# Kernel optimization log

Hardware: AMD Instinct MI355X
Metric: run time of the kernel (lower is better)

The kernel has to match this reference:

```python
import jax, jax.numpy as jnp
from jax import lax
import numpy as np

B, S, H = 4, 4096, 1024
NH, HD, L = 8, 128, 64
EPS = 1e-8


def setup_inputs() -> dict:
    key = jax.random.key(0)
    ks = jax.random.split(key, 11)
    std = 0.02
    d = NH * HD
    return {
        "f_in": jax.random.normal(ks[0], (B, S, H), jnp.float32),
        "i_in": jax.random.normal(ks[1], (B, S, H), jnp.float32),
        "z_in": jax.random.normal(ks[2], (B, S, H), jnp.float32),
        "o_in": jax.random.normal(ks[3], (B, S, H), jnp.float32),
        "c0": jax.random.normal(ks[4], (B, NH, HD), jnp.float32),
        "h0": jax.random.normal(ks[5], (B, NH, HD), jnp.float32),
        "Wf": jax.random.normal(ks[6], (d, H), jnp.float32) * std,
        "bf": jnp.zeros((d,), jnp.float32),
        "Wi": jax.random.normal(ks[7], (d, H), jnp.float32) * std,
        "bi": jnp.zeros((d,), jnp.float32),
        "Wz": jax.random.normal(ks[8], (d, H), jnp.float32) * std,
        "bz": jnp.zeros((d,), jnp.float32),
        "Wo": jax.random.normal(ks[9], (d, H), jnp.float32) * std,
        "bo": jnp.zeros((d,), jnp.float32),
        "Wp": jax.random.normal(ks[10], (H, d), jnp.float32) * std,
        "bp": jnp.zeros((H,), jnp.float32),
    }


def _to_blocks(x):
    # (B,S,NH*HD) -> (n_blocks, B, NH, HD, L)
    nb = S // L
    return x.reshape(B, nb, L, NH, HD).transpose(1, 0, 3, 4, 2)


def reference(f_in, i_in, z_in, o_in, c0, h0, Wf, bf, Wi, bi, Wz, bz, Wo, bo, Wp, bp):
    fx = _to_blocks(f_in @ Wf.T + bf)
    ix = _to_blocks(i_in @ Wi.T + bi)
    zx = _to_blocks(z_in @ Wz.T + bz)
    ox = _to_blocks(o_in @ Wo.T + bo)

    f = jax.nn.sigmoid(fx + 1.0)            # (nb,B,NH,HD,L)
    o = jax.nn.sigmoid(ox)
    upd = jax.nn.sigmoid(ix) * jnp.tanh(zx)

    k = jnp.arange(L)[:, None]
    l = jnp.arange(L + 1)[None, :]
    ones_mask = l >= k + 1                   # set to 1 before cumulative log-prod
    zeros_mask = l >= k + 2                  # strictly-future entries zeroed

    def block_step(c, blk):
        fb, ub, ob = blk                     # each (B,NH,HD,L)
        cf = jnp.concatenate(
            [fb, jnp.ones(fb.shape[:3] + (1,), fb.dtype)], axis=3)  # (B,NH,HD,L+1)
        Fm = jnp.broadcast_to(cf[:, :, :, None, :], fb.shape[:3] + (L, L + 1))
        Fm = jnp.where(ones_mask, 1.0, Fm)
        # reverse cumulative product in log space (matches torch eps trick)
        Fm = jnp.exp(jnp.flip(jnp.cumsum(jnp.flip(jnp.log(Fm + EPS), -1), -1), -1)) - EPS
        Fm = jnp.where(zeros_mask, 0.0, Fm)  # (B,NH,HD,L,L+1)
        u = jnp.concatenate([c[..., None], ub], axis=3)  # (B,NH,HD,L+1)
        cs = jnp.einsum('bhdkl,bhdl->bhdk', Fm, u)       # (B,NH,HD,L)
        hs = ob * jnp.tanh(cs)
        return cs[..., -1], hs

    last_c, hs = lax.scan(block_step, c0, (f, upd, o))   # hs: (nb,B,NH,HD,L)
    last_h = hs[-1][..., -1]
    y = hs.transpose(1, 0, 4, 2, 3).reshape(B, S, NH * HD)
    y = y @ Wp.T + bp                                    # (B,S,H)
    return y, last_c, last_h
```

## Files before the change

### kernel.cpp

```cpp
#include <hip/hip_runtime.h>
#include <hip/hip_bf16.h>
#include <type_traits>

#define GATE_ELEMS 16777216ull
#define W_ELEMS    1048576ull

typedef float f32x4 __attribute__((ext_vector_type(4)));
typedef short s16x8 __attribute__((ext_vector_type(8)));
typedef unsigned short u16;

__device__ __forceinline__ u16 f2bf(float f) {
  union { float f; unsigned u; } v; v.f = f;
  unsigned r = v.u + 0x7fffu + ((v.u >> 16) & 1u);
  return (u16)(r >> 16);
}
__device__ __forceinline__ float bf2f(u16 u) {
  union { unsigned u; float f; } v; v.u = ((unsigned)u) << 16;
  return v.f;
}
__device__ __forceinline__ float sigmoidf_(float x) {
  return 1.0f / (1.0f + __expf(-x));
}
__device__ __forceinline__ float tanhf_(float x) {
  x = fminf(fmaxf(x, -15.f), 15.f);
  const float e = __expf(2.f * x);
  return (e - 1.f) / (e + 1.f);
}

__device__ __forceinline__ void load_lds16(const u16* g, u16* l) {
  __builtin_amdgcn_global_load_lds(
      (const __attribute__((address_space(1))) unsigned int*)g,
      (__attribute__((address_space(3))) unsigned int*)l, 16, 0, 0);
}

#define XCHUNKS 8388608u
#define WCHUNKS 655360u
__global__ void cvt_all(const float* __restrict__ x0, const float* __restrict__ x1,
                        const float* __restrict__ x2, const float* __restrict__ x3,
                        const float* __restrict__ w0, const float* __restrict__ w1,
                        const float* __restrict__ w2, const float* __restrict__ w3,
                        const float* __restrict__ w4,
                        u16* __restrict__ xdst, u16* __restrict__ wdst) {
  const unsigned total = XCHUNKS + WCHUNKS;
  for (unsigned i = blockIdx.x * 256 + threadIdx.x; i < total; i += 2048 * 256) {
    const float* s; u16* d; size_t loc;
    if (i < XCHUNKS) {
      const int w = i >> 21;
      loc = (size_t)(i & 2097151u) * 8;
      s = (w == 0) ? x0 : (w == 1) ? x1 : (w == 2) ? x2 : x3;
      d = xdst + (size_t)w * GATE_ELEMS;
    } else {
      const unsigned j = i - XCHUNKS;
      const int w = j >> 17;
      loc = (size_t)(j & 131071u) * 8;
      s = (w == 0) ? w0 : (w == 1) ? w1 : (w == 2) ? w2 : (w == 3) ? w3 : w4;
      d = wdst + (size_t)w * W_ELEMS;
    }
    const float4 a = *reinterpret_cast<const float4*>(s + loc);
    const float4 b = *reinterpret_cast<const float4*>(s + loc + 4);
    s16x8 wv;
    wv[0] = (short)f2bf(a.x); wv[1] = (short)f2bf(a.y);
    wv[2] = (short)f2bf(a.z); wv[3] = (short)f2bf(a.w);
    wv[4] = (short)f2bf(b.x); wv[5] = (short)f2bf(b.y);
    wv[6] = (short)f2bf(b.z); wv[7] = (short)f2bf(b.w);
    *reinterpret_cast<s16x8*>(d + loc) = wv;
  }
}

__device__ __forceinline__ void stage_mat(const u16* __restrict__ M, int R0, int kt,
                                          u16* ldsbase, int tid) {
#pragma unroll
  for (int l = 0; l < 4; ++l) {
    const int T  = l * 256 + tid;
    const int r  = T >> 3;
    const int sl = (T & 7) ^ (r & 7);
    load_lds16(M + (size_t)(R0 + r) * 1024 + kt + sl * 8,
               ldsbase + (T & ~63) * 8);
  }
}

template <typename OT>
__global__ __launch_bounds__(256, 2)
void gemm_bt128(const u16* __restrict__ A, const u16* __restrict__ Bm,
                const float* __restrict__ bias, OT* __restrict__ C) {
  extern __shared__ u16 lds[];
  const int tid  = threadIdx.x;
  const int lane = tid & 63;
  const int wave = tid >> 6;
  const int wr = wave >> 1;
  const int wc = wave & 1;
  const int frow = lane & 15;
  const int kq   = lane >> 4;

  int bid = blockIdx.x;
  bid = (bid & 7) * 128 + (bid >> 3);
  const int m0 = (bid >> 3) * 128;
  const int n0 = (bid & 7) * 128;

  f32x4 acc[4][4];
#pragma unroll
  for (int i = 0; i < 4; ++i)
#pragma unroll
    for (int j = 0; j < 4; ++j)
      acc[i][j] = (f32x4){0.f, 0.f, 0.f, 0.f};

  stage_mat(A,  m0, 0, lds,        tid);
  stage_mat(Bm, n0, 0, lds + 8192, tid);
  __syncthreads();

  int cur = 0;
#pragma unroll 2
  for (int t = 0; t < 16; ++t) {
    if (t < 15) {
      u16* nb = lds + (cur ^ 1) * 16384;
      stage_mat(A,  m0, (t + 1) * 64, nb,        tid);
      stage_mat(Bm, n0, (t + 1) * 64, nb + 8192, tid);
    }
    const u16* Ab = lds + cur * 16384;
    const u16* Bb = Ab + 8192;
#pragma unroll
    for (int kk = 0; kk < 2; ++kk) {
      s16x8 a[4], b[4];
#pragma unroll
      for (int mf = 0; mf < 4; ++mf) {
        const int r  = wr * 64 + mf * 16 + frow;
        const int ps = (kk * 4 + kq) ^ (r & 7);
        a[mf] = *reinterpret_cast<const s16x8*>(&Ab[r * 64 + ps * 8]);
      }
#pragma unroll
      for (int nf = 0; nf < 4; ++nf) {
        const int r  = wc * 64 + nf * 16 + frow;
        const int ps = (kk * 4 + kq) ^ (r & 7);
        b[nf] = *reinterpret_cast<const s16x8*>(&Bb[r * 64 + ps * 8]);
      }
#pragma unroll
      for (int mf = 0; mf < 4; ++mf)
#pragma unroll
        for (int nf = 0; nf < 4; ++nf)
          acc[mf][nf] = __builtin_amdgcn_mfma_f32_16x16x32_bf16(a[mf], b[nf], acc[mf][nf], 0, 0, 0);
    }
    __syncthreads();
    cur ^= 1;
  }

#pragma unroll
  for (int nf = 0; nf < 4; ++nf) {
    const int col = n0 + wc * 64 + nf * 16 + frow;
    const float bv = bias[col];
#pragma unroll
    for (int mf = 0; mf < 4; ++mf) {
      const int rbase = m0 + wr * 64 + mf * 16 + kq * 4;
#pragma unroll
      for (int r = 0; r < 4; ++r) {
        const float v = acc[mf][nf][r] + bv;
        if constexpr (std::is_same<OT, float>::value)
          C[(size_t)(rbase + r) * 1024 + col] = v;
        else
          C[(size_t)(rbase + r) * 1024 + col] = f2bf(v);
      }
    }
  }
}

__global__ void scan_pass1(const u16* __restrict__ fx, const u16* __restrict__ ix,
                           const u16* __restrict__ zx,
                           float* __restrict__ P, float* __restrict__ cl) {
  const int t  = blockIdx.x * 256 + threadIdx.x;
  const int jg = (t & 255) * 4;
  const int q  = (t >> 8) & 63;
  const int b  = t >> 14;
  const size_t base = ((size_t)(b * 4096 + q * 64)) * 1024 + jg;
  float Pp[4] = {1.f, 1.f, 1.f, 1.f};
  float c[4]  = {0.f, 0.f, 0.f, 0.f};
  for (int s = 0; s < 64; ++s) {
    const size_t o = base + (size_t)s * 1024;
    const ushort4 fv = *reinterpret_cast<const ushort4*>(fx + o);
    const ushort4 iv = *reinterpret_cast<const ushort4*>(ix + o);
    const ushort4 zv = *reinterpret_cast<const ushort4*>(zx + o);
    const u16* fp = (const u16*)&fv;
    const u16* ip = (const u16*)&iv;
    const u16* zp = (const u16*)&zv;
#pragma unroll
    for (int k = 0; k < 4; ++k) {
      const float f = sigmoidf_(bf2f(fp[k]) + 1.f);
      const float u = sigmoidf_(bf2f(ip[k])) * tanhf_(bf2f(zp[k]));
      Pp[k] *= f;
      c[k] = f * c[k] + u;
    }
  }
  const int sidx = q * 4096 + b * 1024 + jg;
  *reinterpret_cast<float4*>(P + sidx)  = make_float4(Pp[0], Pp[1], Pp[2], Pp[3]);
  *reinterpret_cast<float4*>(cl + sidx) = make_float4(c[0], c[1], c[2], c[3]);
}

__global__ void scan_pass2(const float* __restrict__ P, const float* __restrict__ cl,
                           const float* __restrict__ c0, float* __restrict__ cin,
                           float* __restrict__ lastc) {
  const int idx = blockIdx.x * 256 + threadIdx.x;
  float carry = c0[idx];
#pragma unroll
  for (int q = 0; q < 64; ++q) {
    const int s = q * 4096 + idx;
    cin[s] = carry;
    carry = fmaf(P[s], carry, cl[s]);
  }
  lastc[idx] = carry;
}

__global__ void scan_pass3(const u16* __restrict__ fx, const u16* __restrict__ ix,
                           const u16* __restrict__ zx, const u16* __restrict__ ox,
                           const float* __restrict__ cin,
                           u16* __restrict__ h, float* __restrict__ lasth) {
  const int t  = blockIdx.x * 256 + threadIdx.x;
  const int jg = (t & 255) * 4;
  const int q  = (t >> 8) & 63;
  const int b  = t >> 14;
  const size_t base = ((size_t)(b * 4096 + q * 64)) * 1024 + jg;
  const float4 ci = *reinterpret_cast<const float4*>(cin + q * 4096 + b * 1024 + jg);
  float c[4]  = {ci.x, ci.y, ci.z, ci.w};
  float hv[4] = {0.f, 0.f, 0.f, 0.f};
  for (int s = 0; s < 64; ++s) {
    const size_t o = base + (size_t)s * 1024;
    const ushort4 fv = *reinterpret_cast<const ushort4*>(fx + o);
    const ushort4 iv = *reinterpret_cast<const ushort4*>(ix + o);
    const ushort4 zv = *reinterpret_cast<const ushort4*>(zx + o);
    const ushort4 ov = *reinterpret_cast<const ushort4*>(ox + o);
    const u16* fp = (const u16*)&fv;
    const u16* ip = (const u16*)&iv;
    const u16* zp = (const u16*)&zv;
    const u16* op = (const u16*)&ov;
    ushort4 hw;
    u16* hp = (u16*)&hw;
#pragma unroll
    for (int k = 0; k < 4; ++k) {
      const float f = sigmoidf_(bf2f(fp[k]) + 1.f);
      const float u = sigmoidf_(bf2f(ip[k])) * tanhf_(bf2f(zp[k]));
      c[k] = f * c[k] + u;
      hv[k] = sigmoidf_(bf2f(op[k])) * tanhf_(c[k]);
      hp[k] = f2bf(hv[k]);
    }
    *reinterpret_cast<ushort4*>(h + o) = hw;
  }
  if (q == 63)
    *reinterpret_cast<float4*>(lasth + b * 1024 + jg) =
        make_float4(hv[0], hv[1], hv[2], hv[3]);
}

extern "C" void kernel_launch(void* const* d_in, const int* in_sizes, int n_in,
                              void* d_out, int out_size, void* d_ws, size_t ws_size,
                              hipStream_t stream) {
  const float* xin[4]  = {(const float*)d_in[0], (const float*)d_in[1],
                          (const float*)d_in[2], (const float*)d_in[3]};
  const float* c0      = (const float*)d_in[4];
  const float* W[5]    = {(const float*)d_in[6], (const float*)d_in[8],
                          (const float*)d_in[10], (const float*)d_in[12],
                          (const float*)d_in[14]};
  const float* bias[5] = {(const float*)d_in[7], (const float*)d_in[9],
                          (const float*)d_in[11], (const float*)d_in[13],
                          (const float*)d_in[15]};
  float* out = (float*)d_out;

  (void)hipFuncSetAttribute((const void*)gemm_bt128<u16>,
                            hipFuncAttributeMaxDynamicSharedMemorySize, 65536);
  (void)hipFuncSetAttribute((const void*)gemm_bt128<float>,
                            hipFuncAttributeMaxDynamicSharedMemorySize, 65536);

  u16* xbf = (u16*)d_ws;
  u16* wbf = xbf + 4 * GATE_ELEMS;
  float* Pbuf   = (float*)(wbf + 5 * W_ELEMS);
  float* clbuf  = Pbuf + 262144;
  float* cinbuf = clbuf + 262144;

  u16* gp[4];
  gp[0] = (u16*)d_out;
  gp[1] = xbf;
  gp[2] = xbf + GATE_ELEMS;
  gp[3] = xbf + 2 * GATE_ELEMS;
  u16* h = xbf + 3 * GATE_ELEMS;

  cvt_all<<<2048, 256, 0, stream>>>(xin[0], xin[1], xin[2], xin[3],
                                    W[0], W[1], W[2], W[3], W[4], xbf, wbf);

  for (int g = 0; g < 4; ++g)
    gemm_bt128<u16><<<1024, 256, 65536, stream>>>(
        xbf + (size_t)g * GATE_ELEMS, wbf + (size_t)g * W_ELEMS, bias[g], gp[g]);

  scan_pass1<<<256, 256, 0, stream>>>(gp[0], gp[1], gp[2], Pbuf, clbuf);
  scan_pass2<<<16, 256, 0, stream>>>(Pbuf, clbuf, c0, cinbuf, out + GATE_ELEMS);
  scan_pass3<<<256, 256, 0, stream>>>(gp[0], gp[1], gp[2], gp[3], cinbuf, h,
                                      out + GATE_ELEMS + 4096);

  gemm_bt128<float><<<1024, 256, 65536, stream>>>(h, wbf + 4 * W_ELEMS, bias[4], out);
}
```

Baseline: 677.6 us.

## Fuse fp32-to-bf16 activation conversion into gate GEMM and deepen scan parallelism

The separate conversion pass over the four fp32 activation tensors is removed. The gate GEMM now loads fp32 A tiles into registers, converts them with a packed bf16 instruction, and writes them to LDS, overlapping this with the MFMA work on the current tile. This avoids writing and re-reading a 128MB bf16 copy. The scan passes split the sequence into 128 chunks instead of 64 and keep an 8-deep register prefetch ring, giving more parallelism and latency hiding; the cost is more register pressure in the GEMM and a longer serial pass2.

```diff
diff --git a/kernel.cpp b/kernel.cpp
--- a/kernel.cpp
+++ b/kernel.cpp
@@ -4,6 +4,7 @@
 
 #define GATE_ELEMS 16777216ull
 #define W_ELEMS    1048576ull
+#define NQ 128
 
 typedef float f32x4 __attribute__((ext_vector_type(4)));
 typedef short s16x8 __attribute__((ext_vector_type(8)));
@@ -26,49 +27,34 @@
   const float e = __expf(2.f * x);
   return (e - 1.f) / (e + 1.f);
 }
-
+__device__ __forceinline__ unsigned cvtpk(float lo, float hi) {
+  unsigned r;
+  asm("v_cvt_pk_bf16_f32 %0, %1, %2" : "=v"(r) : "v"(lo), "v"(hi));
+  return r;
+}
 __device__ __forceinline__ void load_lds16(const u16* g, u16* l) {
   __builtin_amdgcn_global_load_lds(
       (const __attribute__((address_space(1))) unsigned int*)g,
       (__attribute__((address_space(3))) unsigned int*)l, 16, 0, 0);
 }
 
-#define XCHUNKS 8388608u
-#define WCHUNKS 655360u
-__global__ void cvt_all(const float* __restrict__ x0, const float* __restrict__ x1,
-                        const float* __restrict__ x2, const float* __restrict__ x3,
-                        const float* __restrict__ w0, const float* __restrict__ w1,
-                        const float* __restrict__ w2, const float* __restrict__ w3,
-                        const float* __restrict__ w4,
-                        u16* __restrict__ xdst, u16* __restrict__ wdst) {
-  const unsigned total = XCHUNKS + WCHUNKS;
-  for (unsigned i = blockIdx.x * 256 + threadIdx.x; i < total; i += 2048 * 256) {
-    const float* s; u16* d; size_t loc;
-    if (i < XCHUNKS) {
-      const int w = i >> 21;
-      loc = (size_t)(i & 2097151u) * 8;
-      s = (w == 0) ? x0 : (w == 1) ? x1 : (w == 2) ? x2 : x3;
-      d = xdst + (size_t)w * GATE_ELEMS;
-    } else {
-      const unsigned j = i - XCHUNKS;
-      const int w = j >> 17;
-      loc = (size_t)(j & 131071u) * 8;
-      s = (w == 0) ? w0 : (w == 1) ? w1 : (w == 2) ? w2 : (w == 3) ? w3 : w4;
-      d = wdst + (size_t)w * W_ELEMS;
-    }
-    const float4 a = *reinterpret_cast<const float4*>(s + loc);
-    const float4 b = *reinterpret_cast<const float4*>(s + loc + 4);
-    s16x8 wv;
-    wv[0] = (short)f2bf(a.x); wv[1] = (short)f2bf(a.y);
-    wv[2] = (short)f2bf(a.z); wv[3] = (short)f2bf(a.w);
-    wv[4] = (short)f2bf(b.x); wv[5] = (short)f2bf(b.y);
-    wv[6] = (short)f2bf(b.z); wv[7] = (short)f2bf(b.w);
-    *reinterpret_cast<s16x8*>(d + loc) = wv;
-  }
-}
-
-__device__ __forceinline__ void stage_mat(const u16* __restrict__ M, int R0, int kt,
-                                          u16* ldsbase, int tid) {
+__global__ void cvt_w_kernel(const float* __restrict__ w0, const float* __restrict__ w1,
+                             const float* __restrict__ w2, const float* __restrict__ w3,
+                             const float* __restrict__ w4, u16* __restrict__ dst) {
+  const float* src = (blockIdx.y == 0) ? w0 : (blockIdx.y == 1) ? w1
+                   : (blockIdx.y == 2) ? w2 : (blockIdx.y == 3) ? w3 : w4;
+  u16* d = dst + (size_t)blockIdx.y * W_ELEMS;
+  const size_t i = ((size_t)blockIdx.x * 256 + threadIdx.x) * 8;
+  const float4 a = *reinterpret_cast<const float4*>(src + i);
+  const float4 b = *reinterpret_cast<const float4*>(src + i + 4);
+  uint4 q;
+  q.x = cvtpk(a.x, a.y); q.y = cvtpk(a.z, a.w);
+  q.z = cvtpk(b.x, b.y); q.w = cvtpk(b.z, b.w);
+  *reinterpret_cast<uint4*>(d + i) = q;
+}
+
+__device__ __forceinline__ void stage_bf16(const u16* __restrict__ M, int R0, int kt,
+                                           u16* ldsbase, int tid) {
 #pragma unroll
   for (int l = 0; l < 4; ++l) {
     const int T  = l * 256 + tid;
@@ -78,34 +64,128 @@
                ldsbase + (T & ~63) * 8);
   }
 }
-
-template <typename OT>
+__device__ __forceinline__ void a_issue(const float* __restrict__ A, int m0, int kt,
+                                        int tid, float4 (&av)[8]) {
+  const float* p = A + (size_t)(m0 + (tid >> 3)) * 1024 + kt + (tid & 7) * 8;
+#pragma unroll
+  for (int l = 0; l < 4; ++l) {
+    av[2 * l]     = *reinterpret_cast<const float4*>(p + (size_t)l * 32 * 1024);
+    av[2 * l + 1] = *reinterpret_cast<const float4*>(p + (size_t)l * 32 * 1024 + 4);
+  }
+}
+__device__ __forceinline__ void a_write(u16* Abuf, int tid, const float4 (&av)[8]) {
+  const int rb = tid >> 3, s = tid & 7;
+#pragma unroll
+  for (int l = 0; l < 4; ++l) {
+    const int r  = rb + l * 32;
+    const int ps = s ^ (r & 7);
+    uint4 q;
+    q.x = cvtpk(av[2 * l].x,     av[2 * l].y);
+    q.y = cvtpk(av[2 * l].z,     av[2 * l].w);
+    q.z = cvtpk(av[2 * l + 1].x, av[2 * l + 1].y);
+    q.w = cvtpk(av[2 * l + 1].z, av[2 * l + 1].w);
+    *reinterpret_cast<uint4*>(&Abuf[r * 64 + ps * 8]) = q;
+  }
+}
+
+#define MFMA_BLOCK(Ab, Bb)                                                        \
+  _Pragma("unroll")                                                               \
+  for (int kk = 0; kk < 2; ++kk) {                                                \
+    s16x8 a[4], b[4];                                                             \
+    _Pragma("unroll")                                                             \
+    for (int mf = 0; mf < 4; ++mf) {                                              \
+      const int r  = wr * 64 + mf * 16 + frow;                                    \
+      const int ps = (kk * 4 + kq) ^ (r & 7);                                     \
+      a[mf] = *reinterpret_cast<const s16x8*>(&(Ab)[r * 64 + ps * 8]);            \
+    }                                                                             \
+    _Pragma("unroll")                                                             \
+    for (int nf = 0; nf < 4; ++nf) {                                              \
+      const int r  = wc * 64 + nf * 16 + frow;                                    \
+      const int ps = (kk * 4 + kq) ^ (r & 7);                                     \
+      b[nf] = *reinterpret_cast<const s16x8*>(&(Bb)[r * 64 + ps * 8]);            \
+    }                                                                             \
+    _Pragma("unroll")                                                             \
+    for (int mf = 0; mf < 4; ++mf)                                                \
+      _Pragma("unroll")                                                           \
+      for (int nf = 0; nf < 4; ++nf)                                              \
+        acc[mf][nf] = __builtin_amdgcn_mfma_f32_16x16x32_bf16(a[mf], b[nf],       \
+                                                              acc[mf][nf], 0, 0, 0); \
+  }
+
+#define GEMM_PRE()                                                                \
+  const int tid  = threadIdx.x;                                                   \
+  const int lane = tid & 63;                                                      \
+  const int wave = tid >> 6;                                                      \
+  const int wr = wave >> 1, wc = wave & 1;                                        \
+  const int frow = lane & 15, kq = lane >> 4;                                     \
+  int bid = blockIdx.x;                                                           \
+  bid = (bid & 7) * 128 + (bid >> 3);                                             \
+  const int m0 = (bid >> 3) * 128;                                                \
+  const int n0 = (bid & 7) * 128;                                                 \
+  f32x4 acc[4][4];                                                                \
+  _Pragma("unroll")                                                               \
+  for (int i = 0; i < 4; ++i)                                                     \
+    _Pragma("unroll")                                                             \
+    for (int j = 0; j < 4; ++j)                                                   \
+      acc[i][j] = (f32x4){0.f, 0.f, 0.f, 0.f};
+
+#define GEMM_EPI(C, OT)                                                           \
+  _Pragma("unroll")                                                               \
+  for (int nf = 0; nf < 4; ++nf) {                                                \
+    const int col = n0 + wc * 64 + nf * 16 + frow;                                \
+    const float bv = bias[col];                                                   \
+    _Pragma("unroll")                                                             \
+    for (int mf = 0; mf < 4; ++mf) {                                              \
+      const int rbase = m0 + wr * 64 + mf * 16 + kq * 4;                          \
+      _Pragma("unroll")                                                           \
+      for (int r = 0; r < 4; ++r) {                                               \
+        const float v = acc[mf][nf][r] + bv;                                      \
+        if constexpr (std::is_same<OT, float>::value)                             \
+          (C)[(size_t)(rbase + r) * 1024 + col] = v;                              \
+        else                                                                      \
+          (C)[(size_t)(rbase + r) * 1024 + col] = f2bf(v);                        \
+      }                                                                           \
+    }                                                                             \
+  }
+
 __global__ __launch_bounds__(256, 2)
-void gemm_bt128(const u16* __restrict__ A, const u16* __restrict__ Bm,
-                const float* __restrict__ bias, OT* __restrict__ C) {
+void gemm_gate(const float* __restrict__ A, const u16* __restrict__ Bm,
+               const float* __restrict__ bias, u16* __restrict__ C) {
   extern __shared__ u16 lds[];
-  const int tid  = threadIdx.x;
-  const int lane = tid & 63;
-  const int wave = tid >> 6;
-  const int wr = wave >> 1;
-  const int wc = wave & 1;
-  const int frow = lane & 15;
-  const int kq   = lane >> 4;
-
-  int bid = blockIdx.x;
-  bid = (bid & 7) * 128 + (bid >> 3);
-  const int m0 = (bid >> 3) * 128;
-  const int n0 = (bid & 7) * 128;
-
-  f32x4 acc[4][4];
-#pragma unroll
-  for (int i = 0; i < 4; ++i)
-#pragma unroll
-    for (int j = 0; j < 4; ++j)
-      acc[i][j] = (f32x4){0.f, 0.f, 0.f, 0.f};
-
-  stage_mat(A,  m0, 0, lds,        tid);
-  stage_mat(Bm, n0, 0, lds + 8192, tid);
+  GEMM_PRE();
+
+  float4 av[8];
+  a_issue(A, m0, 0, tid, av);
+  stage_bf16(Bm, n0, 0, lds + 8192, tid);
+  a_write(lds, tid, av);
+  __syncthreads();
+
+  int cur = 0;
+#pragma unroll 2
+  for (int t = 0; t < 16; ++t) {
+    u16* nb = lds + (cur ^ 1) * 16384;
+    if (t < 15) {
+      a_issue(A, m0, (t + 1) * 64, tid, av);
+      stage_bf16(Bm, n0, (t + 1) * 64, nb + 8192, tid);
+    }
+    const u16* Ab = lds + cur * 16384;
+    const u16* Bb = Ab + 8192;
+    MFMA_BLOCK(Ab, Bb);
+    if (t < 15) a_write(nb, tid, av);
+    __syncthreads();
+    cur ^= 1;
+  }
+  GEMM_EPI(C, u16);
+}
+
+__global__ __launch_bounds__(256, 2)
+void gemm_out(const u16* __restrict__ A, const u16* __restrict__ Bm,
+              const float* __restrict__ bias, float* __restrict__ C) {
+  extern __shared__ u16 lds[];
+  GEMM_PRE();
+
+  stage_bf16(A,  m0, 0, lds,        tid);
+  stage_bf16(Bm, n0, 0, lds + 8192, tid);
   __syncthreads();
 
   int cur = 0;
@@ -113,53 +193,16 @@
   for (int t = 0; t < 16; ++t) {
     if (t < 15) {
       u16* nb = lds + (cur ^ 1) * 16384;
-      stage_mat(A,  m0, (t + 1) * 64, nb,        tid);
-      stage_mat(Bm, n0, (t + 1) * 64, nb + 8192, tid);
+      stage_bf16(A,  m0, (t + 1) * 64, nb,        tid);
+      stage_bf16(Bm, n0, (t + 1) * 64, nb + 8192, tid);
     }
     const u16* Ab = lds + cur * 16384;
     const u16* Bb = Ab + 8192;
-#pragma unroll
-    for (int kk = 0; kk < 2; ++kk) {
-      s16x8 a[4], b[4];
-#pragma unroll
-      for (int mf = 0; mf < 4; ++mf) {
-        const int r  = wr * 64 + mf * 16 + frow;
-        const int ps = (kk * 4 + kq) ^ (r & 7);
-        a[mf] = *reinterpret_cast<const s16x8*>(&Ab[r * 64 + ps * 8]);
-      }
-#pragma unroll
-      for (int nf = 0; nf < 4; ++nf) {
-        const int r  = wc * 64 + nf * 16 + frow;
-        const int ps = (kk * 4 + kq) ^ (r & 7);
-        b[nf] = *reinterpret_cast<const s16x8*>(&Bb[r * 64 + ps * 8]);
-      }
-#pragma unroll
-      for (int mf = 0; mf < 4; ++mf)
-#pragma unroll
-        for (int nf = 0; nf < 4; ++nf)
-          acc[mf][nf] = __builtin_amdgcn_mfma_f32_16x16x32_bf16(a[mf], b[nf], acc[mf][nf], 0, 0, 0);
-    }
+    MFMA_BLOCK(Ab, Bb);
     __syncthreads();
     cur ^= 1;
   }
-
-#pragma unroll
-  for (int nf = 0; nf < 4; ++nf) {
-    const int col = n0 + wc * 64 + nf * 16 + frow;
-    const float bv = bias[col];
-#pragma unroll
-    for (int mf = 0; mf < 4; ++mf) {
-      const int rbase = m0 + wr * 64 + mf * 16 + kq * 4;
-#pragma unroll
-      for (int r = 0; r < 4; ++r) {
-        const float v = acc[mf][nf][r] + bv;
-        if constexpr (std::is_same<OT, float>::value)
-          C[(size_t)(rbase + r) * 1024 + col] = v;
-        else
-          C[(size_t)(rbase + r) * 1024 + col] = f2bf(v);
-      }
-    }
-  }
+  GEMM_EPI(C, float);
 }
 
 __global__ void scan_pass1(const u16* __restrict__ fx, const u16* __restrict__ ix,
@@ -167,16 +210,29 @@
                            float* __restrict__ P, float* __restrict__ cl) {
   const int t  = blockIdx.x * 256 + threadIdx.x;
   const int jg = (t & 255) * 4;
-  const int q  = (t >> 8) & 63;
-  const int b  = t >> 14;
-  const size_t base = ((size_t)(b * 4096 + q * 64)) * 1024 + jg;
+  const int q  = (t >> 8) & 127;
+  const int b  = t >> 15;
+  const size_t base = ((size_t)(b * 4096 + q * 32)) * 1024 + jg;
+
+  ushort4 pf[8], pi[8], pz[8];
+#pragma unroll
+  for (int d = 0; d < 8; ++d) {
+    const size_t o = base + (size_t)d * 1024;
+    pf[d] = *reinterpret_cast<const ushort4*>(fx + o);
+    pi[d] = *reinterpret_cast<const ushort4*>(ix + o);
+    pz[d] = *reinterpret_cast<const ushort4*>(zx + o);
+  }
   float Pp[4] = {1.f, 1.f, 1.f, 1.f};
   float c[4]  = {0.f, 0.f, 0.f, 0.f};
-  for (int s = 0; s < 64; ++s) {
-    const size_t o = base + (size_t)s * 1024;
-    const ushort4 fv = *reinterpret_cast<const ushort4*>(fx + o);
-    const ushort4 iv = *reinterpret_cast<const ushort4*>(ix + o);
-    const ushort4 zv = *reinterpret_cast<const ushort4*>(zx + o);
+#pragma unroll
+  for (int s = 0; s < 32; ++s) {
+    const ushort4 fv = pf[s & 7], iv = pi[s & 7], zv = pz[s & 7];
+    if (s + 8 < 32) {
+      const size_t o = base + (size_t)(s + 8) * 1024;
+      pf[s & 7] = *reinterpret_cast<const ushort4*>(fx + o);
+      pi[s & 7] = *reinterpret_cast<const ushort4*>(ix + o);
+      pz[s & 7] = *reinterpret_cast<const ushort4*>(zx + o);
+    }
     const u16* fp = (const u16*)&fv;
     const u16* ip = (const u16*)&iv;
     const u16* zp = (const u16*)&zv;
@@ -198,8 +254,8 @@
                            float* __restrict__ lastc) {
   const int idx = blockIdx.x * 256 + threadIdx.x;
   float carry = c0[idx];
-#pragma unroll
-  for (int q = 0; q < 64; ++q) {
+#pragma unroll 8
+  for (int q = 0; q < NQ; ++q) {
     const int s = q * 4096 + idx;
     cin[s] = carry;
     carry = fmaf(P[s], carry, cl[s]);
@@ -213,18 +269,32 @@
                            u16* __restrict__ h, float* __restrict__ lasth) {
   const int t  = blockIdx.x * 256 + threadIdx.x;
   const int jg = (t & 255) * 4;
-  const int q  = (t >> 8) & 63;
-  const int b  = t >> 14;
-  const size_t base = ((size_t)(b * 4096 + q * 64)) * 1024 + jg;
+  const int q  = (t >> 8) & 127;
+  const int b  = t >> 15;
+  const size_t base = ((size_t)(b * 4096 + q * 32)) * 1024 + jg;
+
+  ushort4 pf[8], pi[8], pz[8], po[8];
+#pragma unroll
+  for (int d = 0; d < 8; ++d) {
+    const size_t o = base + (size_t)d * 1024;
+    pf[d] = *reinterpret_cast<const ushort4*>(fx + o);
+    pi[d] = *reinterpret_cast<const ushort4*>(ix + o);
+    pz[d] = *reinterpret_cast<const ushort4*>(zx + o);
+    po[d] = *reinterpret_cast<const ushort4*>(ox + o);
+  }
   const float4 ci = *reinterpret_cast<const float4*>(cin + q * 4096 + b * 1024 + jg);
   float c[4]  = {ci.x, ci.y, ci.z, ci.w};
   float hv[4] = {0.f, 0.f, 0.f, 0.f};
-  for (int s = 0; s < 64; ++s) {
-    const size_t o = base + (size_t)s * 1024;
-    const ushort4 fv = *reinterpret_cast<const ushort4*>(fx + o);
-    const ushort4 iv = *reinterpret_cast<const ushort4*>(ix + o);
-    const ushort4 zv = *reinterpret_cast<const ushort4*>(zx + o);
-    const ushort4 ov = *reinterpret_cast<const ushort4*>(ox + o);
+#pragma unroll
+  for (int s = 0; s < 32; ++s) {
+    const ushort4 fv = pf[s & 7], iv = pi[s & 7], zv = pz[s & 7], ov = po[s & 7];
+    if (s + 8 < 32) {
+      const size_t o = base + (size_t)(s + 8) * 1024;
+      pf[s & 7] = *reinterpret_cast<const ushort4*>(fx + o);
+      pi[s & 7] = *reinterpret_cast<const ushort4*>(ix + o);
+      pz[s & 7] = *reinterpret_cast<const ushort4*>(zx + o);
+      po[s & 7] = *reinterpret_cast<const ushort4*>(ox + o);
+    }
     const u16* fp = (const u16*)&fv;
     const u16* ip = (const u16*)&iv;
     const u16* zp = (const u16*)&zv;
@@ -239,9 +309,9 @@
       hv[k] = sigmoidf_(bf2f(op[k])) * tanhf_(c[k]);
       hp[k] = f2bf(hv[k]);
     }
-    *reinterpret_cast<ushort4*>(h + o) = hw;
-  }
-  if (q == 63)
+    *reinterpret_cast<ushort4*>(h + base + (size_t)s * 1024) = hw;
+  }
+  if (q == NQ - 1)
     *reinterpret_cast<float4*>(lasth + b * 1024 + jg) =
         make_float4(hv[0], hv[1], hv[2], hv[3]);
 }
@@ -260,35 +330,32 @@
                           (const float*)d_in[15]};
   float* out = (float*)d_out;
 
-  (void)hipFuncSetAttribute((const void*)gemm_bt128<u16>,
+  (void)hipFuncSetAttribute((const void*)gemm_gate,
                             hipFuncAttributeMaxDynamicSharedMemorySize, 65536);
-  (void)hipFuncSetAttribute((const void*)gemm_bt128<float>,
+  (void)hipFuncSetAttribute((const void*)gemm_out,
                             hipFuncAttributeMaxDynamicSharedMemorySize, 65536);
 
-  u16* xbf = (u16*)d_ws;
-  u16* wbf = xbf + 4 * GATE_ELEMS;
+  u16* g1 = (u16*)d_ws;
+  u16* g2 = g1 + GATE_ELEMS;
+  u16* g3 = g2 + GATE_ELEMS;
+  u16* h  = g3 + GATE_ELEMS;
+  u16* wbf = h + GATE_ELEMS;
   float* Pbuf   = (float*)(wbf + 5 * W_ELEMS);
-  float* clbuf  = Pbuf + 262144;
-  float* cinbuf = clbuf + 262144;
-
-  u16* gp[4];
-  gp[0] = (u16*)d_out;
-  gp[1] = xbf;
-  gp[2] = xbf + GATE_ELEMS;
-  gp[3] = xbf + 2 * GATE_ELEMS;
-  u16* h = xbf + 3 * GATE_ELEMS;
-
-  cvt_all<<<2048, 256, 0, stream>>>(xin[0], xin[1], xin[2], xin[3],
-                                    W[0], W[1], W[2], W[3], W[4], xbf, wbf);
-
+  float* clbuf  = Pbuf + NQ * 4096;
+  float* cinbuf = clbuf + NQ * 4096;
+  u16* g0 = (u16*)d_out;
+
+  cvt_w_kernel<<<dim3(512, 5), 256, 0, stream>>>(W[0], W[1], W[2], W[3], W[4], wbf);
+
+  u16* gp[4] = {g0, g1, g2, g3};
   for (int g = 0; g < 4; ++g)
-    gemm_bt128<u16><<<1024, 256, 65536, stream>>>(
-        xbf + (size_t)g * GATE_ELEMS, wbf + (size_t)g * W_ELEMS, bias[g], gp[g]);
-
-  scan_pass1<<<256, 256, 0, stream>>>(gp[0], gp[1], gp[2], Pbuf, clbuf);
+    gemm_gate<<<1024, 256, 65536, stream>>>(
+        xin[g], wbf + (size_t)g * W_ELEMS, bias[g], gp[g]);
+
+  scan_pass1<<<512, 256, 0, stream>>>(g0, g1, g2, Pbuf, clbuf);
   scan_pass2<<<16, 256, 0, stream>>>(Pbuf, clbuf, c0, cinbuf, out + GATE_ELEMS);
-  scan_pass3<<<256, 256, 0, stream>>>(gp[0], gp[1], gp[2], gp[3], cinbuf, h,
+  scan_pass3<<<512, 256, 0, stream>>>(g0, g1, g2, g3, cinbuf, h,
                                       out + GATE_ELEMS + 4096);
 
-  gemm_bt128<float><<<1024, 256, 65536, stream>>>(h, wbf + 4 * W_ELEMS, bias[4], out);
-}
+  gemm_out<<<1024, 256, 65536, stream>>>(h, wbf + 4 * W_ELEMS, bias[4], out);
+}
```

Measured after the change: 945.0 us. 39.5% more time.
